# Kernel optimization log

Measured on AMD Instinct MI355X. Metric: run time of the kernel, lower is better.

The kernel has to match this reference:

```python
import jax, jax.numpy as jnp
import numpy as np
from math import factorial

ZS = np.array([0, 1])
NZ = 2
N_BASIS = 3
N_CHAN = N_BASIS * N_BASIS
N_RBF = 8
MAX_L = 3
CUTOFF = 5.5
P_CUT = 6
N_NODES = 10000
N_EDGES = 100000


def _lxlylz_list(max_l):
    out = []
    for l in range(max_l + 1):
        for lx in range(l, -1, -1):
            for ly in range(l - lx, -1, -1):
                out.append((lx, ly, l - lx - ly))
    return out

LXLYLZ = np.array(_lxlylz_list(MAX_L), dtype=np.int32)  # [n_ang, 3]; (0,0,0) is index 0
N_ANG = LXLYLZ.shape[0]  # 20 for max_l=3

# nu=2 rotational invariants: for each l>0, monomial indices with lx+ly+lz==l and multinomial prefactors
NU2 = []
for l in range(1, MAX_L + 1):
    idx = [i for i in range(N_ANG) if int(LXLYLZ[i].sum()) == l]
    pref = np.array([factorial(l) / (factorial(int(LXLYLZ[i][0])) * factorial(int(LXLYLZ[i][1])) * factorial(int(LXLYLZ[i][2]))) for i in idx], dtype=np.float32)
    NU2.append((np.array(idx, dtype=np.int32), pref))


def setup_inputs() -> dict:
    key = jax.random.key(0)
    ks = jax.random.split(key, 6)
    positions = jax.random.normal(ks[0], (N_NODES, 3), jnp.float32)
    atomic_numbers = jax.random.randint(ks[1], (N_NODES,), 0, NZ)
    edge_index = jax.random.randint(ks[2], (2, N_EDGES), 0, N_NODES)
    edge_lengths = jax.random.uniform(ks[3], (N_EDGES,), jnp.float32, 0.5, CUTOFF)
    edge_vectors = jax.random.normal(ks[4], (N_EDGES, 3), jnp.float32)
    W_embed = jax.random.normal(ks[5], (NZ, N_BASIS), jnp.float32) / np.sqrt(NZ)
    return dict(positions=positions, atomic_numbers=atomic_numbers, edge_index=edge_index,
                edge_lengths=edge_lengths, edge_vectors=edge_vectors, W_embed=W_embed)


def reference(positions, atomic_numbers, edge_index, edge_lengths, edge_vectors, W_embed):
    n_nodes = positions.shape[0]
    # node one-hot over zs -> linear embedding
    one_hot = (atomic_numbers[:, None] == jnp.asarray(ZS)[None, :]).astype(W_embed.dtype)
    emb = one_hot @ W_embed  # [N, n_basis]
    # directed edge-type encoding: outer product of sender/receiver embeddings
    enc = (emb[edge_index[0]][:, :, None] * emb[edge_index[1]][:, None, :]).reshape(-1, N_CHAN)  # [E, c]
    # Bessel radial basis * polynomial cutoff
    r = edge_lengths
    n = jnp.arange(1, N_RBF + 1, dtype=r.dtype)
    radial = jnp.sqrt(2.0 / CUTOFF) * jnp.sin(n[None, :] * jnp.pi * r[:, None] / CUTOFF) / r[:, None]
    u = r / CUTOFF
    p = P_CUT
    fc = (1.0 - 0.5 * (p + 1) * (p + 2) * u ** p + p * (p + 2) * u ** (p + 1)
          - 0.5 * p * (p + 1) * u ** (p + 2)) * (u < 1.0)
    radial = radial * fc[:, None]  # [E, n_rbf]
    # angular monomials x^lx y^ly z^lz of unit edge vectors
    unit = edge_vectors / jnp.linalg.norm(edge_vectors, axis=-1, keepdims=True)
    ang = jnp.prod(unit[:, None, :] ** jnp.asarray(LXLYLZ)[None, :, :], axis=-1)  # [E, n_ang]
    # fused 3-tensor edge product then scatter-sum to receiver nodes
    edge_attr = jnp.einsum('er,ea,ec->erac', radial, ang, enc)  # [E, n_rbf, n_ang, c]
    A = jax.ops.segment_sum(edge_attr, edge_index[1], num_segments=n_nodes)  # node_feat_A
    # symmetrize to invariants: nu=1 (l=0 monomial) + nu=2 per-l invariants
    feats = [A[:, :, 0:1, :]]
    for idx, pref in NU2:
        sel = A[:, :, jnp.asarray(idx), :]
        feats.append(jnp.sum(jnp.asarray(pref)[None, None, :, None] * sel * sel, axis=2, keepdims=True))
    B = jnp.concatenate(feats, axis=2)  # node_feat_B: [N, n_rbf, 1+max_l, c]
    return B
```

## Files before the change

kernel.cpp:

```cpp
#include <hip/hip_runtime.h>


#define NN    10000
#define NE    100000
#define NRBF  8
#define NANG  20
#define NCHAN 9
#define CAP   64
#define CHUNK 16
#define BROW  40
#define NODE_T 192
#define INV_CUT  (1.0f/5.5f)
#define PI_F     3.14159265358979323846f
#define RAD_NORM 0.6030226891555273f

__launch_bounds__(256, 4)
__global__ void edge_k(const int* __restrict__ an, const int* __restrict__ ei,
                       const float* __restrict__ elen, const float* __restrict__ evec,
                       const float* __restrict__ W, int* __restrict__ cnt,
                       int* __restrict__ lst, float* __restrict__ gB)
{
    const int e = blockIdx.x * blockDim.x + threadIdx.x;
    if (e >= NE) return;

    const int src = ei[e];
    const int dst = ei[NE + e];

    const int pos = atomicAdd(&cnt[dst], 1);
    if (pos < CAP) lst[dst * CAP + pos] = e;

    const float r  = elen[e];
    const float vx = evec[3*e+0], vy = evec[3*e+1], vz = evec[3*e+2];
    const float inv = rsqrtf(vx*vx + vy*vy + vz*vz);
    const float x = vx*inv, y = vy*inv, z = vz*inv;

    const float u  = r * INV_CUT;
    const float u2 = u*u, u6 = u2*u2*u2;
    const float fc = (u < 1.0f) ? (1.0f - 28.0f*u6 + 48.0f*u6*u - 21.0f*u6*u2) : 0.0f;
    const float scale = RAD_NORM * fc / r;
    float s1, c1;
    sincosf(PI_F * u, &s1, &c1);
    const float twoc = 2.0f * c1;
    float sp = 0.0f, s = s1;
    float rad[8];
    #pragma unroll
    for (int k = 0; k < 8; ++k) {
        rad[k] = scale * s;
        const float sn = twoc * s - sp;
        sp = s; s = sn;
    }

    const float xx = x*x, xy = x*y, xz = x*z, yy = y*y, yz = y*z, zz = z*z;

    const int zs = an[src], zd = an[dst];
    const float ws0 = W[zs*3+0], ws1 = W[zs*3+1], ws2 = W[zs*3+2];
    const float wd0 = W[zd*3+0], wd1 = W[zd*3+1], wd2 = W[zd*3+2];

    float4* G = (float4*)(gB + (long)e * BROW);
    G[0] = make_float4(rad[0], rad[1], rad[2], rad[3]);
    G[1] = make_float4(rad[4], rad[5], rad[6], rad[7]);
    G[2] = make_float4(1.0f, x, y, z);
    G[3] = make_float4(xx, xy, xz, yy);
    G[4] = make_float4(yz, zz, x*xx, y*xx);
    G[5] = make_float4(z*xx, x*yy, x*yz, x*zz);
    G[6] = make_float4(y*yy, z*yy, y*zz, z*zz);
    G[7] = make_float4(ws0*wd0, ws0*wd1, ws0*wd2, ws1*wd0);
    G[8] = make_float4(ws1*wd1, ws1*wd2, ws2*wd0, ws2*wd1);
    G[9] = make_float4(ws2*wd2, 0.0f, 0.0f, 0.0f);
}

__launch_bounds__(NODE_T, 8)
__global__ void node_k(const int* __restrict__ cnt, const int* __restrict__ lst,
                       const float* __restrict__ gB, float* __restrict__ out)
{
    __shared__ float sB[CHUNK * BROW];
    __shared__ float sA[NRBF * NANG * NCHAN];

    const int n   = blockIdx.x;
    const int tid = threadIdx.x;

    int deg = cnt[n]; if (deg > CAP) deg = CAP;

    const int a_own = tid / 9;
    const int c_own = tid - a_own * 9;
    float acc[8] = {0.f,0.f,0.f,0.f,0.f,0.f,0.f,0.f};

    for (int base = 0; base < deg; base += CHUNK) {
        const int m = min(CHUNK, deg - base);

        for (int i = tid; i < m * BROW; i += NODE_T) {
            const int e = i / BROW;
            const int d = i - e * BROW;
            const int eid = lst[n * CAP + base + e];
            sB[i] = gB[(long)eid * BROW + d];
        }
        __syncthreads();

        if (tid < NANG * NCHAN) {
            for (int e = 0; e < m; ++e) {
                const float* B = &sB[e * BROW];
                const float pe = B[8 + a_own] * B[28 + c_own];
                const float4 r0 = *(const float4*)&B[0];
                const float4 r1 = *(const float4*)&B[4];
                acc[0] = fmaf(r0.x, pe, acc[0]);
                acc[1] = fmaf(r0.y, pe, acc[1]);
                acc[2] = fmaf(r0.z, pe, acc[2]);
                acc[3] = fmaf(r0.w, pe, acc[3]);
                acc[4] = fmaf(r1.x, pe, acc[4]);
                acc[5] = fmaf(r1.y, pe, acc[5]);
                acc[6] = fmaf(r1.z, pe, acc[6]);
                acc[7] = fmaf(r1.w, pe, acc[7]);
            }
        }
        __syncthreads();
    }

    if (tid < NANG * NCHAN) {
        #pragma unroll
        for (int r = 0; r < NRBF; ++r) sA[r * 180 + tid] = acc[r];
    }
    __syncthreads();

    for (int o = tid; o < NRBF*4*NCHAN; o += NODE_T) {
        const int r = o / 36, rem = o - r*36, l = rem / 9, c = rem - (rem/9)*9;
        const float* Ar = &sA[r * 180 + c];
        float val;
        if (l == 0) {
            val = Ar[0];
        } else if (l == 1) {
            const float v1 = Ar[9], v2 = Ar[18], v3 = Ar[27];
            val = v1*v1 + v2*v2 + v3*v3;
        } else if (l == 2) {
            const float v0=Ar[36], v1=Ar[45], v2=Ar[54],
                        v3=Ar[63], v4=Ar[72], v5=Ar[81];
            val = v0*v0 + 2.0f*(v1*v1 + v2*v2 + v4*v4) + v3*v3 + v5*v5;
        } else {
            const float w0=Ar[90],  w1=Ar[99],  w2=Ar[108], w3=Ar[117], w4=Ar[126];
            const float w5=Ar[135], w6=Ar[144], w7=Ar[153], w8=Ar[162], w9=Ar[171];
            val = w0*w0 + w6*w6 + w9*w9
                + 3.0f*(w1*w1 + w2*w2 + w3*w3 + w5*w5 + w7*w7 + w8*w8)
                + 6.0f*w4*w4;
        }
        out[n * (NRBF*4*NCHAN) + o] = val;
    }
}

extern "C" void kernel_launch(void* const* d_in, const int* in_sizes, int n_in,
                              void* d_out, int out_size, void* d_ws, size_t ws_size,
                              hipStream_t stream) {
    const int*   an   = (const int*)d_in[1];
    const int*   ei   = (const int*)d_in[2];
    const float* elen = (const float*)d_in[3];
    const float* evec = (const float*)d_in[4];
    const float* W    = (const float*)d_in[5];
    float* out = (float*)d_out;

    int*   cnt = (int*)d_ws;
    int*   lst = cnt + NN;
    float* gB  = (float*)(lst + (size_t)NN * CAP);

    hipMemsetAsync(cnt, 0, NN * sizeof(int), stream);
    edge_k<<<(NE + 255)/256, 256, 0, stream>>>(an, ei, elen, evec, W, cnt, lst, gB);
    node_k<<<NN, NODE_T, 0, stream>>>(cnt, lst, gB, out);
}
```

Measured before the change: 105.0 us.

## Fuse per-edge feature computation into node kernel, drop global edge buffer

The edge kernel now only bins edges by receiver and packs the sender's atomic number into the list entry. The node kernel recomputes the radial, angular and embedding features for each incoming edge directly into shared memory, one thread per edge. It runs one 64-thread wavefront per node, with each thread holding three angular-channel accumulators. This removes the 160-byte-per-edge global write and gather of the intermediate buffer. In exchange each block has fewer threads, more registers per thread, and a serialized accumulation loop, and it relies on edge ids fitting in 20 bits and degree at most 64.

```diff
diff --git a/kernel.cpp b/kernel.cpp
--- a/kernel.cpp
+++ b/kernel.cpp
@@ -7,121 +7,124 @@
 #define NANG  20
 #define NCHAN 9
 #define CAP   64
-#define CHUNK 16
-#define BROW  40
-#define NODE_T 192
+#define BROW  44
 #define INV_CUT  (1.0f/5.5f)
 #define PI_F     3.14159265358979323846f
 #define RAD_NORM 0.6030226891555273f
 
 __launch_bounds__(256, 4)
-__global__ void edge_k(const int* __restrict__ an, const int* __restrict__ ei,
-                       const float* __restrict__ elen, const float* __restrict__ evec,
-                       const float* __restrict__ W, int* __restrict__ cnt,
-                       int* __restrict__ lst, float* __restrict__ gB)
-{
-    const int e = blockIdx.x * blockDim.x + threadIdx.x;
+__global__ void scatter_k(const int* __restrict__ an, const int* __restrict__ ei,
+                          int* __restrict__ cnt, int* __restrict__ lst) {
+    int e = blockIdx.x * blockDim.x + threadIdx.x;
     if (e >= NE) return;
-
-    const int src = ei[e];
-    const int dst = ei[NE + e];
-
-    const int pos = atomicAdd(&cnt[dst], 1);
-    if (pos < CAP) lst[dst * CAP + pos] = e;
-
-    const float r  = elen[e];
-    const float vx = evec[3*e+0], vy = evec[3*e+1], vz = evec[3*e+2];
-    const float inv = rsqrtf(vx*vx + vy*vy + vz*vz);
-    const float x = vx*inv, y = vy*inv, z = vz*inv;
-
-    const float u  = r * INV_CUT;
-    const float u2 = u*u, u6 = u2*u2*u2;
-    const float fc = (u < 1.0f) ? (1.0f - 28.0f*u6 + 48.0f*u6*u - 21.0f*u6*u2) : 0.0f;
-    const float scale = RAD_NORM * fc / r;
-    float s1, c1;
-    sincosf(PI_F * u, &s1, &c1);
-    const float twoc = 2.0f * c1;
-    float sp = 0.0f, s = s1;
-    float rad[8];
-    #pragma unroll
-    for (int k = 0; k < 8; ++k) {
-        rad[k] = scale * s;
-        const float sn = twoc * s - sp;
-        sp = s; s = sn;
-    }
-
-    const float xx = x*x, xy = x*y, xz = x*z, yy = y*y, yz = y*z, zz = z*z;
-
-    const int zs = an[src], zd = an[dst];
-    const float ws0 = W[zs*3+0], ws1 = W[zs*3+1], ws2 = W[zs*3+2];
-    const float wd0 = W[zd*3+0], wd1 = W[zd*3+1], wd2 = W[zd*3+2];
-
-    float4* G = (float4*)(gB + (long)e * BROW);
-    G[0] = make_float4(rad[0], rad[1], rad[2], rad[3]);
-    G[1] = make_float4(rad[4], rad[5], rad[6], rad[7]);
-    G[2] = make_float4(1.0f, x, y, z);
-    G[3] = make_float4(xx, xy, xz, yy);
-    G[4] = make_float4(yz, zz, x*xx, y*xx);
-    G[5] = make_float4(z*xx, x*yy, x*yz, x*zz);
-    G[6] = make_float4(y*yy, z*yy, y*zz, z*zz);
-    G[7] = make_float4(ws0*wd0, ws0*wd1, ws0*wd2, ws1*wd0);
-    G[8] = make_float4(ws1*wd1, ws1*wd2, ws2*wd0, ws2*wd1);
-    G[9] = make_float4(ws2*wd2, 0.0f, 0.0f, 0.0f);
+    int src = ei[e];
+    int dst = ei[NE + e];
+    int zs  = an[src];
+    int pos = atomicAdd(&cnt[dst], 1);
+    if (pos < CAP) lst[dst * CAP + pos] = e | (zs << 20);
 }
 
-__launch_bounds__(NODE_T, 8)
-__global__ void node_k(const int* __restrict__ cnt, const int* __restrict__ lst,
-                       const float* __restrict__ gB, float* __restrict__ out)
+__launch_bounds__(64, 4)
+__global__ void node_k(const int* __restrict__ an, const float* __restrict__ elen,
+                       const float* __restrict__ evec, const float* __restrict__ W,
+                       const int* __restrict__ cnt, const int* __restrict__ lst,
+                       float* __restrict__ out)
 {
-    __shared__ float sB[CHUNK * BROW];
-    __shared__ float sA[NRBF * NANG * NCHAN];
+    __shared__ float sB[CAP * BROW];
+    float* sA = sB;
 
     const int n   = blockIdx.x;
     const int tid = threadIdx.x;
 
     int deg = cnt[n]; if (deg > CAP) deg = CAP;
+    const int zd = an[n];
 
-    const int a_own = tid / 9;
-    const int c_own = tid - a_own * 9;
-    float acc[8] = {0.f,0.f,0.f,0.f,0.f,0.f,0.f,0.f};
+    const float W0=W[0], W1=W[1], W2=W[2], W3=W[3], W4=W[4], W5=W[5];
+    const float wd0 = zd ? W3 : W0, wd1 = zd ? W4 : W1, wd2 = zd ? W5 : W2;
 
-    for (int base = 0; base < deg; base += CHUNK) {
-        const int m = min(CHUNK, deg - base);
+    if (tid < deg) {
+        const int v   = lst[n * CAP + tid];
+        const int eid = v & 0xFFFFF;
+        const int zs  = v >> 20;
 
-        for (int i = tid; i < m * BROW; i += NODE_T) {
-            const int e = i / BROW;
-            const int d = i - e * BROW;
-            const int eid = lst[n * CAP + base + e];
-            sB[i] = gB[(long)eid * BROW + d];
+        const float r  = elen[eid];
+        const float vx = evec[3*eid+0], vy = evec[3*eid+1], vz = evec[3*eid+2];
+        const float inv = rsqrtf(vx*vx + vy*vy + vz*vz);
+        const float x = vx*inv, y = vy*inv, z = vz*inv;
+
+        const float u  = r * INV_CUT;
+        const float u2 = u*u, u6 = u2*u2*u2;
+        const float fc = (u < 1.0f) ? (1.0f - 28.0f*u6 + 48.0f*u6*u - 21.0f*u6*u2)
+                                    : 0.0f;
+        const float scale = RAD_NORM * fc / r;
+        float s1, c1;
+        sincosf(PI_F * u, &s1, &c1);
+        const float twoc = 2.0f * c1;
+        float sp = 0.0f, s = s1;
+        float rad[8];
+        #pragma unroll
+        for (int k = 0; k < 8; ++k) {
+            rad[k] = scale * s;
+            const float sn = twoc * s - sp;
+            sp = s; s = sn;
         }
-        __syncthreads();
 
-        if (tid < NANG * NCHAN) {
-            for (int e = 0; e < m; ++e) {
-                const float* B = &sB[e * BROW];
-                const float pe = B[8 + a_own] * B[28 + c_own];
-                const float4 r0 = *(const float4*)&B[0];
-                const float4 r1 = *(const float4*)&B[4];
-                acc[0] = fmaf(r0.x, pe, acc[0]);
-                acc[1] = fmaf(r0.y, pe, acc[1]);
-                acc[2] = fmaf(r0.z, pe, acc[2]);
-                acc[3] = fmaf(r0.w, pe, acc[3]);
-                acc[4] = fmaf(r1.x, pe, acc[4]);
-                acc[5] = fmaf(r1.y, pe, acc[5]);
-                acc[6] = fmaf(r1.z, pe, acc[6]);
-                acc[7] = fmaf(r1.w, pe, acc[7]);
-            }
-        }
-        __syncthreads();
-    }
+        const float xx = x*x, xy = x*y, xz = x*z, yy = y*y, yz = y*z, zz = z*z;
+        const float ws0 = zs ? W3 : W0, ws1 = zs ? W4 : W1, ws2 = zs ? W5 : W2;
 
-    if (tid < NANG * NCHAN) {
-        #pragma unroll
-        for (int r = 0; r < NRBF; ++r) sA[r * 180 + tid] = acc[r];
+        float* B = &sB[tid * BROW];
+        *(float4*)&B[0]  = make_float4(rad[0], rad[1], rad[2], rad[3]);
+        *(float4*)&B[4]  = make_float4(rad[4], rad[5], rad[6], rad[7]);
+        *(float4*)&B[8]  = make_float4(1.0f, x, y, z);
+        *(float4*)&B[12] = make_float4(xx, xy, xz, yy);
+        *(float4*)&B[16] = make_float4(yz, zz, x*xx, y*xx);
+        *(float4*)&B[20] = make_float4(z*xx, x*yy, x*yz, x*zz);
+        *(float4*)&B[24] = make_float4(y*yy, z*yy, y*zz, z*zz);
+        *(float4*)&B[28] = make_float4(ws0*wd0, ws0*wd1, ws0*wd2, ws1*wd0);
+        *(float4*)&B[32] = make_float4(ws1*wd1, ws1*wd2, ws2*wd0, ws2*wd1);
+        B[36] = ws2*wd2;
     }
     __syncthreads();
 
-    for (int o = tid; o < NRBF*4*NCHAN; o += NODE_T) {
+    const int a0 = tid / 9,          c0 = tid - 9*a0;
+    const int p1 = tid + 64,  a1 = p1 / 9, c1 = p1 - 9*a1;
+    const int p2 = tid + 128, a2 = (tid < 52) ? p2 / 9 : 0,
+                              c2 = (tid < 52) ? p2 - 9*(p2/9) : 0;
+    float acc0[8] = {0,0,0,0,0,0,0,0};
+    float acc1[8] = {0,0,0,0,0,0,0,0};
+    float acc2[8] = {0,0,0,0,0,0,0,0};
+
+    for (int e = 0; e < deg; ++e) {
+        const float* B = &sB[e * BROW];
+        const float4 r0 = *(const float4*)&B[0];
+        const float4 r1 = *(const float4*)&B[4];
+        const float pe0 = B[8 + a0] * B[28 + c0];
+        const float pe1 = B[8 + a1] * B[28 + c1];
+        const float pe2 = B[8 + a2] * B[28 + c2];
+        acc0[0]=fmaf(r0.x,pe0,acc0[0]); acc0[1]=fmaf(r0.y,pe0,acc0[1]);
+        acc0[2]=fmaf(r0.z,pe0,acc0[2]); acc0[3]=fmaf(r0.w,pe0,acc0[3]);
+        acc0[4]=fmaf(r1.x,pe0,acc0[4]); acc0[5]=fmaf(r1.y,pe0,acc0[5]);
+        acc0[6]=fmaf(r1.z,pe0,acc0[6]); acc0[7]=fmaf(r1.w,pe0,acc0[7]);
+        acc1[0]=fmaf(r0.x,pe1,acc1[0]); acc1[1]=fmaf(r0.y,pe1,acc1[1]);
+        acc1[2]=fmaf(r0.z,pe1,acc1[2]); acc1[3]=fmaf(r0.w,pe1,acc1[3]);
+        acc1[4]=fmaf(r1.x,pe1,acc1[4]); acc1[5]=fmaf(r1.y,pe1,acc1[5]);
+        acc1[6]=fmaf(r1.z,pe1,acc1[6]); acc1[7]=fmaf(r1.w,pe1,acc1[7]);
+        acc2[0]=fmaf(r0.x,pe2,acc2[0]); acc2[1]=fmaf(r0.y,pe2,acc2[1]);
+        acc2[2]=fmaf(r0.z,pe2,acc2[2]); acc2[3]=fmaf(r0.w,pe2,acc2[3]);
+        acc2[4]=fmaf(r1.x,pe2,acc2[4]); acc2[5]=fmaf(r1.y,pe2,acc2[5]);
+        acc2[6]=fmaf(r1.z,pe2,acc2[6]); acc2[7]=fmaf(r1.w,pe2,acc2[7]);
+    }
+    __syncthreads();
+
+    #pragma unroll
+    for (int r = 0; r < NRBF; ++r) {
+        sA[r*180 + tid] = acc0[r];
+        sA[r*180 + p1]  = acc1[r];
+        if (tid < 52) sA[r*180 + p2] = acc2[r];
+    }
+    __syncthreads();
+
+    for (int o = tid; o < NRBF*4*NCHAN; o += 64) {
         const int r = o / 36, rem = o - r*36, l = rem / 9, c = rem - (rem/9)*9;
         const float* Ar = &sA[r * 180 + c];
         float val;
@@ -155,11 +158,10 @@
     const float* W    = (const float*)d_in[5];
     float* out = (float*)d_out;
 
-    int*   cnt = (int*)d_ws;
-    int*   lst = cnt + NN;
-    float* gB  = (float*)(lst + (size_t)NN * CAP);
+    int* cnt = (int*)d_ws;
+    int* lst = cnt + NN;
 
     hipMemsetAsync(cnt, 0, NN * sizeof(int), stream);
-    edge_k<<<(NE + 255)/256, 256, 0, stream>>>(an, ei, elen, evec, W, cnt, lst, gB);
-    node_k<<<NN, NODE_T, 0, stream>>>(cnt, lst, gB, out);
+    scatter_k<<<(NE + 255)/256, 256, 0, stream>>>(an, ei, cnt, lst);
+    node_k<<<NN, 64, 0, stream>>>(an, elen, evec, W, cnt, lst, out);
 }
```

New measurement: 95.33 us. 9.2% less time.
